# Optimization experiments

Measured on AMD Instinct MI355X. Metric: run time of the kernel, lower is better.

The kernel has to match this reference:

```python
import jax, jax.numpy as jnp
import numpy as np

B, S, ENC, HID = 2, 2048, 2048, 2048
HQ, HKV, D = 8, 4, 256
SOFTCAP = 50.0
SCALING = float(256) ** -0.5  # query_pre_attn_scalar ** -0.5
EPS = 1e-6
NEG = -1e9  # finite stand-in for -inf in additive masks


def _rms_norm(x, w, eps=EPS):
    # GemmaRMSNorm: fp32 compute, scale by (1 + weight)
    xf = x.astype(jnp.float32)
    n = xf * jax.lax.rsqrt(jnp.mean(xf * xf, axis=-1, keepdims=True) + eps)
    return (n * (1.0 + w.astype(jnp.float32))).astype(x.dtype)


def _rotate_half(x):
    x1, x2 = jnp.split(x, 2, axis=-1)
    return jnp.concatenate([-x2, x1], axis=-1)


def _apply_rope(q, k, cos, sin):
    # q,k: [B, H, S, D]; cos,sin: [1, S, D] -> unsqueeze head dim
    c, s = cos[:, None, :, :], sin[:, None, :, :]
    return q * c + _rotate_half(q) * s, k * c + _rotate_half(k) * s


def setup_inputs() -> dict:
    key = jax.random.key(0)
    ks = jax.random.split(key, 8)
    hidden_states = jax.random.normal(ks[0], (B, S, HID), jnp.float32)
    encoder_hidden_states = jax.random.normal(ks[1], (B, ENC, HID), jnp.float32)
    # RoPE tables (base 10000)
    pos = jnp.arange(S, dtype=jnp.float32)
    inv_freq = 1.0 / (10000.0 ** (jnp.arange(0, D, 2, dtype=jnp.float32) / D))
    freqs = pos[:, None] * inv_freq[None, :]                 # [S, D/2]
    emb = jnp.concatenate([freqs, freqs], axis=-1)           # [S, D]
    cos = jnp.cos(emb)[None]                                 # [1, S, D]
    sin = jnp.sin(emb)[None]
    # merged additive mask: causal over self part, fully visible cross part
    causal = jnp.where(jnp.arange(S)[:, None] >= jnp.arange(S)[None, :], 0.0, NEG)
    mask = jnp.concatenate([causal, jnp.zeros((S, ENC), jnp.float32)], axis=-1)
    merged_attention_mask = mask[None, None].astype(jnp.float32)  # [1,1,S,S+ENC]
    w = 0.02
    Wq = jax.random.normal(ks[2], (HQ * D, HID), jnp.float32) * w
    Wk = jax.random.normal(ks[3], (HKV * D, HID), jnp.float32) * w
    Wv = jax.random.normal(ks[4], (HKV * D, HID), jnp.float32) * w
    Wo = jax.random.normal(ks[5], (HID, HQ * D), jnp.float32) * w
    q_norm_w = jnp.zeros((D,), jnp.float32)
    k_norm_w = jnp.zeros((D,), jnp.float32)
    return dict(hidden_states=hidden_states, encoder_hidden_states=encoder_hidden_states,
                cos=cos, sin=sin, merged_attention_mask=merged_attention_mask,
                Wq=Wq, Wk=Wk, Wv=Wv, Wo=Wo, q_norm_w=q_norm_w, k_norm_w=k_norm_w)


def reference(hidden_states, encoder_hidden_states, cos, sin, merged_attention_mask,
              Wq, Wk, Wv, Wo, q_norm_w, k_norm_w):
    b, s, _ = hidden_states.shape
    enc = encoder_hidden_states.shape[1]
    n_rep = HQ // HKV
    # projections
    q = hidden_states @ Wq.T                                 # [B,S,HQ*D]
    k_self = hidden_states @ Wk.T
    v_self = hidden_states @ Wv.T
    k_cross = encoder_hidden_states @ Wk.T
    v_cross = encoder_hidden_states @ Wv.T
    q = q.reshape(b, s, HQ, D).transpose(0, 2, 1, 3)         # [B,HQ,S,D]
    k_self = k_self.reshape(b, s, HKV, D).transpose(0, 2, 1, 3)
    v_self = v_self.reshape(b, s, HKV, D).transpose(0, 2, 1, 3)
    k_cross = k_cross.reshape(b, enc, HKV, D).transpose(0, 2, 1, 3)
    v_cross = v_cross.reshape(b, enc, HKV, D).transpose(0, 2, 1, 3)
    # QK RMSNorm + RoPE (RoPE only on self q/k)
    q = _rms_norm(q, q_norm_w)
    k_self = _rms_norm(k_self, k_norm_w)
    k_cross = _rms_norm(k_cross, k_norm_w)
    q, k_self = _apply_rope(q, k_self, cos, sin)
    # merged KV + GQA repeat
    k = jnp.concatenate([k_self, k_cross], axis=2)           # [B,HKV,S+ENC,D]
    v = jnp.concatenate([v_self, v_cross], axis=2)
    k = jnp.repeat(k, n_rep, axis=1)                         # [B,HQ,S+ENC,D]
    v = jnp.repeat(v, n_rep, axis=1)
    # eager softcapped attention
    scores = jnp.einsum('bhqd,bhkd->bhqk', q, k) * SCALING
    scores = SOFTCAP * jnp.tanh(scores / SOFTCAP)
    scores = scores + merged_attention_mask
    probs = jax.nn.softmax(scores, axis=-1)
    attn = jnp.einsum('bhqk,bhkd->bhqd', probs, v)           # [B,HQ,S,D]
    attn = attn.transpose(0, 2, 1, 3).reshape(b, s, HQ * D)
    return attn @ Wo.T
```

## Files before the change

### kernel.cpp

```cpp
#include <hip/hip_runtime.h>
#include <cstdint>

typedef __attribute__((ext_vector_type(8))) short bf16x8;
typedef __attribute__((ext_vector_type(4))) float f32x4;

#define B_ 2
#define S_ 2048
#define ENC_ 2048
#define HID_ 2048
#define HQ_ 8
#define HKV_ 4
#define D_ 256
#define L_ 4096

__device__ __forceinline__ short f2bf(float f) {
  uint32_t u = __builtin_bit_cast(uint32_t, f);
  u = (u + 0x7fffu + ((u >> 16) & 1u)) >> 16;
  return (short)u;
}
__device__ __forceinline__ float bf2f(short s) {
  uint32_t u = ((uint32_t)(uint16_t)s) << 16;
  return __builtin_bit_cast(float, u);
}

__device__ __forceinline__ void llds16(const void* g, void* s) {
  __builtin_amdgcn_global_load_lds(
      (const __attribute__((address_space(1))) void*)(__builtin_bit_cast(uintptr_t, g)),
      (__attribute__((address_space(3))) void*)(uint32_t)(__builtin_bit_cast(uintptr_t, s)),
      16, 0, 0);
}

__device__ __forceinline__ void wg_barrier() {
  asm volatile("" ::: "memory");
  __builtin_amdgcn_s_barrier();
  asm volatile("" ::: "memory");
}

__global__ __launch_bounds__(256) void cvt_f32_bf16(const float* __restrict__ in,
                                                    short* __restrict__ out, int n) {
  int i = (blockIdx.x * 256 + threadIdx.x) * 4;
  if (i >= n) return;
  float4 v = *(const float4*)(in + i);
  short4 r;
  r.x = f2bf(v.x); r.y = f2bf(v.y); r.z = f2bf(v.z); r.w = f2bf(v.w);
  *(short4*)(out + i) = r;
}

template <int BF16OUT>
__global__ __launch_bounds__(256, 2)
void gemm_bt(const short* __restrict__ A, const short* __restrict__ Bw,
             void* __restrict__ Cout, int M, int N, int K) {
  __shared__ __align__(16) short As[128 * 32];
  __shared__ __align__(16) short Bs[128 * 32];
  const int t = threadIdx.x;
  const int w = t >> 6;
  const int l = t & 63;
  const int lr = l & 15;
  const int lq = l >> 4;
  const int bm = blockIdx.y * 128;
  const int bn = blockIdx.x * 128;
  const int wm = (w & 1) * 64;
  const int wn = (w >> 1) * 64;

  f32x4 acc[4][4];
#pragma unroll
  for (int i = 0; i < 4; i++)
#pragma unroll
    for (int j = 0; j < 4; j++) acc[i][j] = f32x4{0.f, 0.f, 0.f, 0.f};

  const int srow = 32 * w + (l >> 2);
  const int scol = (l & 3) * 8;
  const short* gA = A + (size_t)(bm + srow) * K + scol;
  const short* gB = Bw + (size_t)(bn + srow) * K + scol;
  short* sA = &As[srow * 32 + scol];
  short* sB = &Bs[srow * 32 + scol];

  for (int k0 = 0; k0 < K; k0 += 32) {
    llds16(gA + k0, sA);
    llds16(gA + k0 + (size_t)16 * K, sA + 16 * 32);
    llds16(gB + k0, sB);
    llds16(gB + k0 + (size_t)16 * K, sB + 16 * 32);
    __syncthreads();
    bf16x8 af[4], bfr[4];
#pragma unroll
    for (int mi = 0; mi < 4; mi++)
      af[mi] = *(const bf16x8*)&As[(wm + 16 * mi + lr) * 32 + lq * 8];
#pragma unroll
    for (int ni = 0; ni < 4; ni++)
      bfr[ni] = *(const bf16x8*)&Bs[(wn + 16 * ni + lr) * 32 + lq * 8];
    __syncthreads();
#pragma unroll
    for (int mi = 0; mi < 4; mi++)
#pragma unroll
      for (int ni = 0; ni < 4; ni++)
        acc[mi][ni] =
            __builtin_amdgcn_mfma_f32_16x16x32_bf16(af[mi], bfr[ni], acc[mi][ni], 0, 0, 0);
  }

#pragma unroll
  for (int mi = 0; mi < 4; mi++)
#pragma unroll
    for (int ni = 0; ni < 4; ni++)
#pragma unroll
      for (int r = 0; r < 4; r++) {
        int row = bm + wm + 16 * mi + lq * 4 + r;
        int col = bn + wn + 16 * ni + lr;
        float v = acc[mi][ni][r];
        if (BF16OUT)
          ((short*)Cout)[(size_t)row * N + col] = f2bf(v);
        else
          ((float*)Cout)[(size_t)row * N + col] = v;
      }
}

__global__ __launch_bounds__(256)
void norm_rope(const short* __restrict__ src, int src_ld, int col0, int H,
               short* __restrict__ dst, int dstL, int pos_off, int do_rope, int kswz,
               const float* __restrict__ wn, const float* __restrict__ cosp,
               const float* __restrict__ sinp) {
  __shared__ float sh[256];
  __shared__ float red[4];
  int bid = blockIdx.x;
  int s = bid & (S_ - 1);
  int h = (bid >> 11) % H;
  int b = (bid >> 11) / H;
  int d = threadIdx.x;
  int w = d >> 6, l = d & 63;
  float x = bf2f(src[(size_t)(b * S_ + s) * src_ld + col0 + h * D_ + d]);
  float ss = x * x;
#pragma unroll
  for (int off = 32; off; off >>= 1) ss += __shfl_xor(ss, off, 64);
  if (l == 0) red[w] = ss;
  __syncthreads();
  float tot = red[0] + red[1] + red[2] + red[3];
  float y = x * rsqrtf(tot * (1.0f / D_) + 1e-6f) * (1.0f + wn[d]);
  float outv = y;
  if (do_rope) {
    sh[d] = y;
    __syncthreads();
    float c = cosp[s * D_ + d];
    float sn = sinp[s * D_ + d];
    outv = (d < 128) ? (y * c - sh[d + 128] * sn) : (y * c + sh[d - 128] * sn);
  }
  int dd = d;
  if (kswz) dd = (((d >> 3) ^ (s & 7)) << 3) | (d & 7);
  dst[((size_t)(b * H + h) * dstL + pos_off + s) * D_ + dd] = f2bf(outv);
}

__global__ __launch_bounds__(256)
void v_transpose(const short* __restrict__ qkv_self, const short* __restrict__ kv_cross,
                 short* __restrict__ Vt) {
  __shared__ __align__(16) short tile[64][72];
  int bid = blockIdx.x;
  int dt = bid & 3;
  int lt = (bid >> 2) & 63;
  int h = (bid >> 8) & 3;
  int b = bid >> 10;
  int t = threadIdx.x;
  int rl = t >> 2;
  int cc = (t & 3) * 16;
  int l = lt * 64 + rl;
  const short* src;
  if (lt < 32)
    src = qkv_self + (size_t)(b * S_ + l) * 4096 + 3072 + h * D_ + dt * 64 + cc;
  else
    src = kv_cross + (size_t)(b * ENC_ + (l - S_)) * 2048 + 1024 + h * D_ + dt * 64 + cc;
  *(bf16x8*)&tile[rl][cc] = *(const bf16x8*)src;
  *(bf16x8*)&tile[rl][cc + 8] = *(const bf16x8*)(src + 8);
  __syncthreads();
  int dl = t >> 2;
  int lc = (t & 3) * 16;
  bf16x8 v0, v1;
#pragma unroll
  for (int j = 0; j < 8; j++) {
    v0[j] = tile[lc + j][dl];
    v1[j] = tile[lc + 8 + j][dl];
  }
  int d = dt * 64 + dl;
  int e3 = (dl >> 1) & 3;
  int c0 = 2 * (t & 3);
  int c1 = c0 + 1;
  int p0 = (c0 & 4) | ((c0 ^ e3) & 3);
  int p1 = (c1 & 4) | ((c1 ^ e3) & 3);
  short* rowp = Vt + ((size_t)(b * HKV_ + h) * D_ + d) * (size_t)L_ + lt * 64;
  *(bf16x8*)(rowp + p0 * 8) = v0;
  *(bf16x8*)(rowp + p1 * 8) = v1;
}

__global__ __launch_bounds__(256, 2)
void flash_attn(const short* __restrict__ Q, const short* __restrict__ K,
                const short* __restrict__ Vt, short* __restrict__ part0,
                short* __restrict__ part1, short* __restrict__ part2,
                short* __restrict__ part3, float* __restrict__ lsum) {
  __shared__ __align__(16) short Ks[2][32 * 256];
  __shared__ __align__(16) short Vs[2][256 * 32];
  __shared__ __align__(16) short Ps[4][2][16 * 40];
  int t = threadIdx.x, w = t >> 6, l = t & 63;
  int lr = l & 15, lq = l >> 4, x7 = lr & 7, vx = (lr >> 1) & 3;
  int bid = blockIdx.x;
  int pair = bid >> 6;
  int p = (bid >> 4) & 3;
  int bh = bid & 15;
  int b = bh >> 3, h = bh & 7, hk = h >> 1;
  short* op = (p == 0) ? part0 : (p == 1) ? part1 : (p == 2) ? part2 : part3;

  const short* Kbase = K + (size_t)(b * HKV_ + hk) * L_ * D_;
  const short* Vbase = Vt + (size_t)(b * HKV_ + hk) * (size_t)D_ * L_;

  auto stage = [&](int bufi, int k0) {
    const short* kg = Kbase + (size_t)(k0 + 8 * w + (l >> 5)) * 256 + (l & 31) * 8;
    short* ks = &Ks[bufi][8 * w * 256 + l * 8];
#pragma unroll
    for (int i = 0; i < 4; i++) llds16(kg + i * 512, ks + i * 512);
    const short* vg = Vbase + (size_t)(64 * w + (l >> 2)) * (size_t)L_ + k0 + (l & 3) * 8;
    short* vs = &Vs[bufi][64 * w * 32 + l * 8];
#pragma unroll
    for (int i = 0; i < 4; i++) llds16(vg + (size_t)(16 * i) * L_, vs + i * 512);
  };

  int gi = p;
  const int lenA = 2 * pair + 34;

  for (int phase = 0; phase < 2; ++phase) {
    int qt = phase ? (15 - pair) : pair;
    int q0 = qt * 128;
    int nself = 2 * qt + 2;
    int base = phase ? lenA : 0;
    int lim = base + nself + 32;
    int qg0 = q0 + 32 * w + lr;
    int qg1 = qg0 + 16;

    bf16x8 qf0[8], qf1[8];
    {
      const short* qb0 = Q + ((size_t)(b * HQ_ + h) * S_ + qg0) * D_ + lq * 8;
      const short* qb1 = qb0 + (size_t)16 * D_;
#pragma unroll
      for (int kf = 0; kf < 8; kf++) {
        qf0[kf] = *(const bf16x8*)(qb0 + kf * 32);
        qf1[kf] = *(const bf16x8*)(qb1 + kf * 32);
      }
    }
    f32x4 o0[16], o1[16];
#pragma unroll
    for (int i = 0; i < 16; i++) {
      o0[i] = f32x4{0.f, 0.f, 0.f, 0.f};
      o1[i] = f32x4{0.f, 0.f, 0.f, 0.f};
    }
    float lacc0 = 0.f, lacc1 = 0.f;

    int gcur = gi, u = 0, buf = 0;
    {
      int local = gcur - base;
      int j = (local < nself) ? local : (local - nself + 32);
      stage(0, j * 64);
    }

    while (true) {
      int gn = gcur, un = u + 1;
      if (un == 2) { un = 0; gn = gcur + 4; }
      bool hn = (gn < lim);
      if (hn) {
        int localn = gn - base;
        int jn = (localn < nself) ? localn : (localn - nself + 32);
        stage(buf ^ 1, jn * 64 + 32 * un);
        asm volatile("s_waitcnt vmcnt(8)" ::: "memory");
      } else {
        asm volatile("s_waitcnt vmcnt(0)" ::: "memory");
      }
      wg_barrier();

      int local = gcur - base;
      int j = (local < nself) ? local : (local - nself + 32);
      int k0 = j * 64 + 32 * u;
      bool diag = (local >= nself - 2) && (local < nself);
      const short* KsB = &Ks[buf][0];
      const short* VsB = &Vs[buf][0];

      f32x4 sc[2][2];
#pragma unroll
      for (int nt = 0; nt < 2; nt++) {
        sc[nt][0] = f32x4{0.f, 0.f, 0.f, 0.f};
        sc[nt][1] = f32x4{0.f, 0.f, 0.f, 0.f};
      }
      __builtin_amdgcn_s_setprio(1);
#pragma unroll
      for (int kf = 0; kf < 8; kf++) {
#pragma unroll
        for (int nt = 0; nt < 2; nt++) {
          bf16x8 a = *(const bf16x8*)&KsB[(nt * 16 + lr) * 256 + (((4 * kf + lq) ^ x7) * 8)];
          sc[nt][0] = __builtin_amdgcn_mfma_f32_16x16x32_bf16(a, qf0[kf], sc[nt][0], 0, 0, 0);
          sc[nt][1] = __builtin_amdgcn_mfma_f32_16x16x32_bf16(a, qf1[kf], sc[nt][1], 0, 0, 0);
        }
      }
      __builtin_amdgcn_s_setprio(0);

      auto softcap_store = [&](const f32x4& s4, int keybase, int qg, float& lacc,
                               int qh, int nt) {
        float pe[4];
#pragma unroll
        for (int r = 0; r < 4; r++) {
          float s = s4[r];
          float t2 = s * s * 1.5625e-6f;
          float hh = fmaf(t2, -0.0033730157f, 0.0083333338f);
          hh = fmaf(t2, hh, -0.020833334f);
          hh = fmaf(t2, hh, 0.0625f);
          float cap = s * hh;
          float pv = __expf(cap);
          if (diag && (keybase + 4 * lq + r > qg)) pv = 0.f;
          pe[r] = pv;
        }
        lacc += (pe[0] + pe[1]) + (pe[2] + pe[3]);
        uint32_t lo = (uint32_t)(uint16_t)f2bf(pe[0]) | ((uint32_t)(uint16_t)f2bf(pe[1]) << 16);
        uint32_t hi = (uint32_t)(uint16_t)f2bf(pe[2]) | ((uint32_t)(uint16_t)f2bf(pe[3]) << 16);
        *(uint2*)&Ps[w][qh][lr * 40 + nt * 16 + lq * 4] = uint2{lo, hi};
      };
      softcap_store(sc[0][0], k0, qg0, lacc0, 0, 0);
      softcap_store(sc[1][0], k0 + 16, qg0, lacc0, 0, 1);
      softcap_store(sc[0][1], k0, qg1, lacc1, 1, 0);
      softcap_store(sc[1][1], k0 + 16, qg1, lacc1, 1, 1);

      bf16x8 pb0 = *(const bf16x8*)&Ps[w][0][lr * 40 + lq * 8];
      bf16x8 pb1 = *(const bf16x8*)&Ps[w][1][lr * 40 + lq * 8];
      __builtin_amdgcn_s_setprio(1);
#pragma unroll
      for (int dt = 0; dt < 16; dt++) {
        bf16x8 va = *(const bf16x8*)&VsB[(dt * 16 + lr) * 32 + ((lq ^ vx) * 8)];
        o0[dt] = __builtin_amdgcn_mfma_f32_16x16x32_bf16(va, pb0, o0[dt], 0, 0, 0);
        o1[dt] = __builtin_amdgcn_mfma_f32_16x16x32_bf16(va, pb1, o1[dt], 0, 0, 0);
      }
      __builtin_amdgcn_s_setprio(0);

      wg_barrier();
      if (!hn) break;
      gcur = gn; u = un; buf ^= 1;
    }
    gi = gcur + 4;

    size_t orow0 = ((size_t)b * S_ + qg0) * (HQ_ * D_) + h * D_;
    size_t orow1 = orow0 + (size_t)16 * (HQ_ * D_);
#pragma unroll
    for (int dt = 0; dt < 16; dt++) {
      short4 st;
      st.x = f2bf(o0[dt][0]);
      st.y = f2bf(o0[dt][1]);
      st.z = f2bf(o0[dt][2]);
      st.w = f2bf(o0[dt][3]);
      *(short4*)(op + orow0 + dt * 16 + 4 * lq) = st;
      st.x = f2bf(o1[dt][0]);
      st.y = f2bf(o1[dt][1]);
      st.z = f2bf(o1[dt][2]);
      st.w = f2bf(o1[dt][3]);
      *(short4*)(op + orow1 + dt * 16 + 4 * lq) = st;
    }
    float lrow0 = lacc0, lrow1 = lacc1;
    lrow0 += __shfl_xor(lrow0, 16, 64);
    lrow0 += __shfl_xor(lrow0, 32, 64);
    lrow1 += __shfl_xor(lrow1, 16, 64);
    lrow1 += __shfl_xor(lrow1, 32, 64);
    if (lq == 0) {
      size_t lb = (((size_t)p * B_ + b) * HQ_ + h) * S_;
      lsum[lb + qg0] = lrow0;
      lsum[lb + qg1] = lrow1;
    }
  }
}

__global__ __launch_bounds__(256)
void combine4(const short* __restrict__ p0, const short* __restrict__ p1,
              const short* __restrict__ p2, const short* __restrict__ p3,
              const float* __restrict__ lsum, short* __restrict__ out) {
  int tid = blockIdx.x * 256 + threadIdx.x;
  size_t flat = (size_t)tid * 4;
  int h = ((int)(flat >> 8)) & 7;
  int s = ((int)(flat >> 11)) & 2047;
  int b = (int)(flat >> 22);
  size_t sbase = ((size_t)b * HQ_ + h) * S_ + s;
  const size_t SP = (size_t)B_ * HQ_ * S_;
  float inv = 1.0f / (lsum[sbase] + lsum[SP + sbase] + lsum[2 * SP + sbase] +
                      lsum[3 * SP + sbase]);
  short4 a = *(const short4*)(p0 + flat);
  short4 c = *(const short4*)(p1 + flat);
  short4 d = *(const short4*)(p2 + flat);
  short4 e = *(const short4*)(p3 + flat);
  short4 r;
  r.x = f2bf((bf2f(a.x) + bf2f(c.x) + bf2f(d.x) + bf2f(e.x)) * inv);
  r.y = f2bf((bf2f(a.y) + bf2f(c.y) + bf2f(d.y) + bf2f(e.y)) * inv);
  r.z = f2bf((bf2f(a.z) + bf2f(c.z) + bf2f(d.z) + bf2f(e.z)) * inv);
  r.w = f2bf((bf2f(a.w) + bf2f(c.w) + bf2f(d.w) + bf2f(e.w)) * inv);
  *(short4*)(out + flat) = r;
}

extern "C" void kernel_launch(void* const* d_in, const int* in_sizes, int n_in, void* d_out,
                              int out_size, void* d_ws, size_t ws_size, hipStream_t stream) {
  (void)in_sizes; (void)n_in; (void)out_size; (void)ws_size;
  const float* hidden = (const float*)d_in[0];
  const float* encoder = (const float*)d_in[1];
  const float* cosp = (const float*)d_in[2];
  const float* sinp = (const float*)d_in[3];
  const float* Wq = (const float*)d_in[5];
  const float* Wk = (const float*)d_in[6];
  const float* Wv = (const float*)d_in[7];
  const float* Wo = (const float*)d_in[8];
  const float* qnw = (const float*)d_in[9];
  const float* knw = (const float*)d_in[10];

  short* ws = (short*)d_ws;
  short* hs_bf = ws;
  short* enc_bf = ws + 8388608;
  short* wqkv_bf = ws + 16777216;
  short* wo_bf = ws + 25165824;
  short* qkv_self = ws + 29360128;
  short* kv_cross = ws + 46137344;
  short* Kb = ws + 54525952;
  short* Vtb = ws + 62914560;
  short* attn_b = hs_bf;
  short* Qb = enc_bf;
  short* part0 = qkv_self;
  short* part1 = qkv_self + 8388608;
  short* part2 = kv_cross;
  short* part3 = wqkv_bf;
  float* lsum = (float*)d_out;

  cvt_f32_bf16<<<8192, 256, 0, stream>>>(hidden, hs_bf, 8388608);
  cvt_f32_bf16<<<8192, 256, 0, stream>>>(encoder, enc_bf, 8388608);
  cvt_f32_bf16<<<4096, 256, 0, stream>>>(Wq, wqkv_bf, 4194304);
  cvt_f32_bf16<<<2048, 256, 0, stream>>>(Wk, wqkv_bf + 4194304, 2097152);
  cvt_f32_bf16<<<2048, 256, 0, stream>>>(Wv, wqkv_bf + 6291456, 2097152);
  cvt_f32_bf16<<<4096, 256, 0, stream>>>(Wo, wo_bf, 4194304);

  gemm_bt<1><<<dim3(32, 32), 256, 0, stream>>>(hs_bf, wqkv_bf, qkv_self, 4096, 4096, 2048);
  gemm_bt<1><<<dim3(16, 32), 256, 0, stream>>>(enc_bf, wqkv_bf + (size_t)2048 * 2048, kv_cross,
                                               4096, 2048, 2048);

  norm_rope<<<32768, 256, 0, stream>>>(qkv_self, 4096, 0, 8, Qb, 2048, 0, 1, 0, qnw, cosp, sinp);
  norm_rope<<<16384, 256, 0, stream>>>(qkv_self, 4096, 2048, 4, Kb, 4096, 0, 1, 1, knw, cosp, sinp);
  norm_rope<<<16384, 256, 0, stream>>>(kv_cross, 2048, 0, 4, Kb, 4096, 2048, 0, 1, knw, cosp, sinp);

  v_transpose<<<2048, 256, 0, stream>>>(qkv_self, kv_cross, Vtb);

  flash_attn<<<512, 256, 0, stream>>>(Qb, Kb, Vtb, part0, part1, part2, part3, lsum);
  combine4<<<16384, 256, 0, stream>>>(part0, part1, part2, part3, lsum, attn_b);

  gemm_bt<0><<<dim3(16, 32), 256, 0, stream>>>(attn_b, wo_bf, d_out, 4096, 2048, 2048);
}
```

Before: 584.5 us.

## Replace GEMM with double-buffered swizzled large-tile kernel and tidy attention inner loop

Replaces the single-buffered 128x128 GEMM with a 512-thread kernel that uses larger tiles (BM up to 256, BN 256), a K-step of 64, double-buffered LDS with async global-to-LDS loads and XOR swizzling, and a block-index remap for L2 locality. The flash attention kernel precomputes LDS offsets and staging pointers, restructures the softcap/exp loop so the causal mask is applied only on diagonal tiles, and uses packed v_cvt_pk_bf16_f32 conversions for P and the output. The aim is to cut GEMM memory stalls and attention VALU overhead. Larger tiles and more LDS per block may reduce occupancy, and the explicit vmcnt values depend on the number of loads issued per stage.

```diff
diff --git a/kernel.cpp b/kernel.cpp
--- a/kernel.cpp
+++ b/kernel.cpp
@@ -22,6 +22,11 @@
   uint32_t u = ((uint32_t)(uint16_t)s) << 16;
   return __builtin_bit_cast(float, u);
 }
+__device__ __forceinline__ uint32_t cvtpk(float lo, float hi) {
+  uint32_t r;
+  asm("v_cvt_pk_bf16_f32 %0, %1, %2" : "=v"(r) : "v"(lo), "v"(hi));
+  return r;
+}
 
 __device__ __forceinline__ void llds16(const void* g, void* s) {
   __builtin_amdgcn_global_load_lds(
@@ -46,59 +51,92 @@
   *(short4*)(out + i) = r;
 }
 
-template <int BF16OUT>
-__global__ __launch_bounds__(256, 2)
-void gemm_bt(const short* __restrict__ A, const short* __restrict__ Bw,
-             void* __restrict__ Cout, int M, int N, int K) {
-  __shared__ __align__(16) short As[128 * 32];
-  __shared__ __align__(16) short Bs[128 * 32];
+template <int BM, int WM, int BF16OUT>
+__global__ __launch_bounds__(512, 2)
+void gemm_ring(const short* __restrict__ A, const short* __restrict__ Bw,
+               void* __restrict__ Cout, int M, int N, int K) {
+  constexpr int BN = 256;
+  constexpr int LA = BM * 8 / 512;
+  constexpr int LB = BN * 8 / 512;
+  constexpr int LTOT = LA + LB;
+  __shared__ __align__(16) short As[2][BM * 64];
+  __shared__ __align__(16) short Bs[2][BN * 64];
   const int t = threadIdx.x;
-  const int w = t >> 6;
-  const int l = t & 63;
-  const int lr = l & 15;
-  const int lq = l >> 4;
-  const int bm = blockIdx.y * 128;
-  const int bn = blockIdx.x * 128;
-  const int wm = (w & 1) * 64;
-  const int wn = (w >> 1) * 64;
-
-  f32x4 acc[4][4];
-#pragma unroll
-  for (int i = 0; i < 4; i++)
-#pragma unroll
-    for (int j = 0; j < 4; j++) acc[i][j] = f32x4{0.f, 0.f, 0.f, 0.f};
-
-  const int srow = 32 * w + (l >> 2);
-  const int scol = (l & 3) * 8;
-  const short* gA = A + (size_t)(bm + srow) * K + scol;
-  const short* gB = Bw + (size_t)(bn + srow) * K + scol;
-  short* sA = &As[srow * 32 + scol];
-  short* sB = &Bs[srow * 32 + scol];
-
-  for (int k0 = 0; k0 < K; k0 += 32) {
-    llds16(gA + k0, sA);
-    llds16(gA + k0 + (size_t)16 * K, sA + 16 * 32);
-    llds16(gB + k0, sB);
-    llds16(gB + k0 + (size_t)16 * K, sB + 16 * 32);
-    __syncthreads();
-    bf16x8 af[4], bfr[4];
-#pragma unroll
-    for (int mi = 0; mi < 4; mi++)
-      af[mi] = *(const bf16x8*)&As[(wm + 16 * mi + lr) * 32 + lq * 8];
-#pragma unroll
-    for (int ni = 0; ni < 4; ni++)
-      bfr[ni] = *(const bf16x8*)&Bs[(wn + 16 * ni + lr) * 32 + lq * 8];
-    __syncthreads();
-#pragma unroll
-    for (int mi = 0; mi < 4; mi++)
+  const int w = t >> 6, l = t & 63;
+  const int lr = l & 15, lq = l >> 4, x7 = lr & 7;
+
+  int nbx = N >> 8;
+  int bid = blockIdx.x;
+  int cpx = gridDim.x >> 3;
+  int wg = (bid & 7) * cpx + (bid >> 3);
+  int by = wg / nbx, bx = wg - (wg / nbx) * nbx;
+  const int bm = by * BM, bn = bx * BN;
+  const int wm = (w & 1) * WM, wn = (w >> 1) * 64;
+
+  uint32_t goffA[LA], soffA[LA], goffB[LB], soffB[LB];
+#pragma unroll
+  for (int i = 0; i < LA; i++) {
+    int slot = i * 512 + t;
+    int row = slot >> 3, cp = slot & 7;
+    goffA[i] = (uint32_t)((bm + row) * K + ((cp ^ (row & 7)) * 8));
+    soffA[i] = (uint32_t)(slot * 8);
+  }
+#pragma unroll
+  for (int i = 0; i < LB; i++) {
+    int slot = i * 512 + t;
+    int row = slot >> 3, cp = slot & 7;
+    goffB[i] = (uint32_t)((bn + row) * K + ((cp ^ (row & 7)) * 8));
+    soffB[i] = (uint32_t)(slot * 8);
+  }
+
+  auto stage = [&](int bufi, int k0) {
+#pragma unroll
+    for (int i = 0; i < LA; i++) llds16(A + (size_t)goffA[i] + k0, &As[bufi][soffA[i]]);
+#pragma unroll
+    for (int i = 0; i < LB; i++) llds16(Bw + (size_t)goffB[i] + k0, &Bs[bufi][soffB[i]]);
+  };
+
+  f32x4 acc[WM / 16][4];
+#pragma unroll
+  for (int mi = 0; mi < WM / 16; mi++)
+#pragma unroll
+    for (int ni = 0; ni < 4; ni++) acc[mi][ni] = f32x4{0.f, 0.f, 0.f, 0.f};
+
+  const int NT = K >> 6;
+  stage(0, 0);
+  for (int tt = 0; tt < NT; tt++) {
+    if (tt + 1 < NT) {
+      stage((tt + 1) & 1, (tt + 1) << 6);
+      if (LTOT == 8)
+        asm volatile("s_waitcnt vmcnt(8)" ::: "memory");
+      else
+        asm volatile("s_waitcnt vmcnt(6)" ::: "memory");
+    } else {
+      asm volatile("s_waitcnt vmcnt(0)" ::: "memory");
+    }
+    wg_barrier();
+    const char* Ab = (const char*)&As[tt & 1][0];
+    const char* Bb = (const char*)&Bs[tt & 1][0];
+#pragma unroll
+    for (int ks = 0; ks < 2; ks++) {
+      const int cof = ((4 * ks + lq) ^ x7) * 16;
+      bf16x8 bfrag[4];
 #pragma unroll
       for (int ni = 0; ni < 4; ni++)
-        acc[mi][ni] =
-            __builtin_amdgcn_mfma_f32_16x16x32_bf16(af[mi], bfr[ni], acc[mi][ni], 0, 0, 0);
-  }
-
-#pragma unroll
-  for (int mi = 0; mi < 4; mi++)
+        bfrag[ni] = *(const bf16x8*)(Bb + (wn + 16 * ni + lr) * 128 + cof);
+#pragma unroll
+      for (int mi = 0; mi < WM / 16; mi++) {
+        bf16x8 af = *(const bf16x8*)(Ab + (wm + 16 * mi + lr) * 128 + cof);
+#pragma unroll
+        for (int ni = 0; ni < 4; ni++)
+          acc[mi][ni] = __builtin_amdgcn_mfma_f32_16x16x32_bf16(af, bfrag[ni], acc[mi][ni], 0, 0, 0);
+      }
+    }
+    wg_barrier();
+  }
+
+#pragma unroll
+  for (int mi = 0; mi < WM / 16; mi++)
 #pragma unroll
     for (int ni = 0; ni < 4; ni++)
 #pragma unroll
@@ -207,13 +245,24 @@
   const short* Kbase = K + (size_t)(b * HKV_ + hk) * L_ * D_;
   const short* Vbase = Vt + (size_t)(b * HKV_ + hk) * (size_t)D_ * L_;
 
+  uint32_t kofs[8];
+#pragma unroll
+  for (int kf = 0; kf < 8; kf++)
+    kofs[kf] = (uint32_t)(lr * 512 + (((4 * kf + lq) ^ x7) * 16));
+  const uint32_t vof = (uint32_t)(lr * 64 + ((lq ^ vx) * 16));
+
+  const short* kg_lane = Kbase + (8 * w + (l >> 5)) * 256 + (l & 31) * 8;
+  const short* vg_lane = Vbase + (size_t)(64 * w + (l >> 2)) * (size_t)L_ + (l & 3) * 8;
+  short* ks_lane = &Ks[0][8 * w * 256 + l * 8];
+  short* vs_lane = &Vs[0][64 * w * 32 + l * 8];
+
   auto stage = [&](int bufi, int k0) {
-    const short* kg = Kbase + (size_t)(k0 + 8 * w + (l >> 5)) * 256 + (l & 31) * 8;
-    short* ks = &Ks[bufi][8 * w * 256 + l * 8];
+    const short* kg = kg_lane + (size_t)k0 * 256;
+    short* ks = ks_lane + bufi * (32 * 256);
 #pragma unroll
     for (int i = 0; i < 4; i++) llds16(kg + i * 512, ks + i * 512);
-    const short* vg = Vbase + (size_t)(64 * w + (l >> 2)) * (size_t)L_ + k0 + (l & 3) * 8;
-    short* vs = &Vs[bufi][64 * w * 32 + l * 8];
+    const short* vg = vg_lane + k0;
+    short* vs = vs_lane + bufi * (256 * 32);
 #pragma unroll
     for (int i = 0; i < 4; i++) llds16(vg + (size_t)(16 * i) * L_, vs + i * 512);
   };
@@ -273,8 +322,8 @@
       int j = (local < nself) ? local : (local - nself + 32);
       int k0 = j * 64 + 32 * u;
       bool diag = (local >= nself - 2) && (local < nself);
-      const short* KsB = &Ks[buf][0];
-      const short* VsB = &Vs[buf][0];
+      const char* KsB = (const char*)&Ks[buf][0];
+      const char* VsB = (const char*)&Vs[buf][0];
 
       f32x4 sc[2][2];
 #pragma unroll
@@ -287,44 +336,55 @@
       for (int kf = 0; kf < 8; kf++) {
 #pragma unroll
         for (int nt = 0; nt < 2; nt++) {
-          bf16x8 a = *(const bf16x8*)&KsB[(nt * 16 + lr) * 256 + (((4 * kf + lq) ^ x7) * 8)];
+          bf16x8 a = *(const bf16x8*)(KsB + kofs[kf] + nt * 8192);
           sc[nt][0] = __builtin_amdgcn_mfma_f32_16x16x32_bf16(a, qf0[kf], sc[nt][0], 0, 0, 0);
           sc[nt][1] = __builtin_amdgcn_mfma_f32_16x16x32_bf16(a, qf1[kf], sc[nt][1], 0, 0, 0);
         }
       }
       __builtin_amdgcn_s_setprio(0);
 
-      auto softcap_store = [&](const f32x4& s4, int keybase, int qg, float& lacc,
-                               int qh, int nt) {
-        float pe[4];
-#pragma unroll
-        for (int r = 0; r < 4; r++) {
-          float s = s4[r];
-          float t2 = s * s * 1.5625e-6f;
-          float hh = fmaf(t2, -0.0033730157f, 0.0083333338f);
-          hh = fmaf(t2, hh, -0.020833334f);
-          hh = fmaf(t2, hh, 0.0625f);
-          float cap = s * hh;
-          float pv = __expf(cap);
-          if (diag && (keybase + 4 * lq + r > qg)) pv = 0.f;
-          pe[r] = pv;
-        }
-        lacc += (pe[0] + pe[1]) + (pe[2] + pe[3]);
-        uint32_t lo = (uint32_t)(uint16_t)f2bf(pe[0]) | ((uint32_t)(uint16_t)f2bf(pe[1]) << 16);
-        uint32_t hi = (uint32_t)(uint16_t)f2bf(pe[2]) | ((uint32_t)(uint16_t)f2bf(pe[3]) << 16);
-        *(uint2*)&Ps[w][qh][lr * 40 + nt * 16 + lq * 4] = uint2{lo, hi};
-      };
-      softcap_store(sc[0][0], k0, qg0, lacc0, 0, 0);
-      softcap_store(sc[1][0], k0 + 16, qg0, lacc0, 0, 1);
-      softcap_store(sc[0][1], k0, qg1, lacc1, 1, 0);
-      softcap_store(sc[1][1], k0 + 16, qg1, lacc1, 1, 1);
+      f32x4 pe[2][2];
+#pragma unroll
+      for (int nt = 0; nt < 2; nt++)
+#pragma unroll
+        for (int qh = 0; qh < 2; qh++)
+#pragma unroll
+          for (int r = 0; r < 4; r++) {
+            float s = sc[nt][qh][r];
+            float t2 = s * s * 1.5625e-6f;
+            float hh = fmaf(t2, -0.0033730157f, 0.0083333338f);
+            hh = fmaf(t2, hh, -0.020833334f);
+            hh = fmaf(t2, hh, 0.0625f);
+            pe[nt][qh][r] = __expf(s * hh);
+          }
+      if (diag) {
+        int kb = k0 + 4 * lq;
+#pragma unroll
+        for (int nt = 0; nt < 2; nt++)
+#pragma unroll
+          for (int r = 0; r < 4; r++) {
+            if (kb + nt * 16 + r > qg0) pe[nt][0][r] = 0.f;
+            if (kb + nt * 16 + r > qg1) pe[nt][1][r] = 0.f;
+          }
+      }
+      lacc0 += (pe[0][0][0] + pe[0][0][1]) + (pe[0][0][2] + pe[0][0][3]) +
+               (pe[1][0][0] + pe[1][0][1]) + (pe[1][0][2] + pe[1][0][3]);
+      lacc1 += (pe[0][1][0] + pe[0][1][1]) + (pe[0][1][2] + pe[0][1][3]) +
+               (pe[1][1][0] + pe[1][1][1]) + (pe[1][1][2] + pe[1][1][3]);
+#pragma unroll
+      for (int nt = 0; nt < 2; nt++) {
+        *(uint2*)&Ps[w][0][lr * 40 + nt * 16 + lq * 4] =
+            uint2{cvtpk(pe[nt][0][0], pe[nt][0][1]), cvtpk(pe[nt][0][2], pe[nt][0][3])};
+        *(uint2*)&Ps[w][1][lr * 40 + nt * 16 + lq * 4] =
+            uint2{cvtpk(pe[nt][1][0], pe[nt][1][1]), cvtpk(pe[nt][1][2], pe[nt][1][3])};
+      }
 
       bf16x8 pb0 = *(const bf16x8*)&Ps[w][0][lr * 40 + lq * 8];
       bf16x8 pb1 = *(const bf16x8*)&Ps[w][1][lr * 40 + lq * 8];
       __builtin_amdgcn_s_setprio(1);
 #pragma unroll
       for (int dt = 0; dt < 16; dt++) {
-        bf16x8 va = *(const bf16x8*)&VsB[(dt * 16 + lr) * 32 + ((lq ^ vx) * 8)];
+        bf16x8 va = *(const bf16x8*)(VsB + vof + dt * 1024);
         o0[dt] = __builtin_amdgcn_mfma_f32_16x16x32_bf16(va, pb0, o0[dt], 0, 0, 0);
         o1[dt] = __builtin_amdgcn_mfma_f32_16x16x32_bf16(va, pb1, o1[dt], 0, 0, 0);
       }
@@ -340,17 +400,10 @@
     size_t orow1 = orow0 + (size_t)16 * (HQ_ * D_);
 #pragma unroll
     for (int dt = 0; dt < 16; dt++) {
-      short4 st;
-      st.x = f2bf(o0[dt][0]);
-      st.y = f2bf(o0[dt][1]);
-      st.z = f2bf(o0[dt][2]);
-      st.w = f2bf(o0[dt][3]);
-      *(short4*)(op + orow0 + dt * 16 + 4 * lq) = st;
-      st.x = f2bf(o1[dt][0]);
-      st.y = f2bf(o1[dt][1]);
-      st.z = f2bf(o1[dt][2]);
-      st.w = f2bf(o1[dt][3]);
-      *(short4*)(op + orow1 + dt * 16 + 4 * lq) = st;
+      *(uint2*)(op + orow0 + dt * 16 + 4 * lq) =
+          uint2{cvtpk(o0[dt][0], o0[dt][1]), cvtpk(o0[dt][2], o0[dt][3])};
+      *(uint2*)(op + orow1 + dt * 16 + 4 * lq) =
+          uint2{cvtpk(o1[dt][0], o1[dt][1]), cvtpk(o1[dt][2], o1[dt][3])};
     }
     float lrow0 = lacc0, lrow1 = lacc1;
     lrow0 += __shfl_xor(lrow0, 16, 64);
@@ -428,9 +481,9 @@
   cvt_f32_bf16<<<2048, 256, 0, stream>>>(Wv, wqkv_bf + 6291456, 2097152);
   cvt_f32_bf16<<<4096, 256, 0, stream>>>(Wo, wo_bf, 4194304);
 
-  gemm_bt<1><<<dim3(32, 32), 256, 0, stream>>>(hs_bf, wqkv_bf, qkv_self, 4096, 4096, 2048);
-  gemm_bt<1><<<dim3(16, 32), 256, 0, stream>>>(enc_bf, wqkv_bf + (size_t)2048 * 2048, kv_cross,
-                                               4096, 2048, 2048);
+  gemm_ring<256, 128, 1><<<256, 512, 0, stream>>>(hs_bf, wqkv_bf, qkv_self, 4096, 4096, 2048);
+  gemm_ring<128, 64, 1><<<256, 512, 0, stream>>>(enc_bf, wqkv_bf + (size_t)2048 * 2048,
+                                                 kv_cross, 4096, 2048, 2048);
 
   norm_rope<<<32768, 256, 0, stream>>>(qkv_self, 4096, 0, 8, Qb, 2048, 0, 1, 0, qnw, cosp, sinp);
   norm_rope<<<16384, 256, 0, stream>>>(qkv_self, 4096, 2048, 4, Kb, 4096, 0, 1, 1, knw, cosp, sinp);
@@ -441,5 +494,5 @@
   flash_attn<<<512, 256, 0, stream>>>(Qb, Kb, Vtb, part0, part1, part2, part3, lsum);
   combine4<<<16384, 256, 0, stream>>>(part0, part1, part2, part3, lsum, attn_b);
 
-  gemm_bt<0><<<dim3(16, 32), 256, 0, stream>>>(attn_b, wo_bf, d_out, 4096, 2048, 2048);
-}
+  gemm_ring<128, 64, 0><<<256, 512, 0, stream>>>(attn_b, wo_bf, d_out, 4096, 2048, 2048);
+}
```

After: 533.0 us. -8.8%, faster.
